# Kernel optimization log

Measured on AMD Instinct MI355X. Metric: run time of the kernel, lower is better.

The kernel has to match this reference:

```python
import jax, jax.numpy as jnp
import numpy as np

TOP_K = 2


def setup_inputs() -> dict:
    key = jax.random.key(0)
    ks = jax.random.split(key, 5)
    T, D, F, E = 2048, 2048, 7168, 8
    x = jax.random.normal(ks[0], (T, D), dtype=jnp.float32)
    gate_w = jax.random.normal(ks[1], (E, D), dtype=jnp.float32) * 0.02
    w1 = jax.random.normal(ks[2], (E, F, D), dtype=jnp.float32) * 0.02
    w3 = jax.random.normal(ks[3], (E, F, D), dtype=jnp.float32) * 0.02
    w2 = jax.random.normal(ks[4], (E, D, F), dtype=jnp.float32) * 0.02
    return {"x": x, "gate_w": gate_w, "w1": w1, "w3": w3, "w2": w2}


def reference(x, gate_w, w1, w3, w2):
    # x: (T, D); gate_w: (E, D); w1/w3: (E, F, D); w2: (E, D, F)
    T = x.shape[0]
    E = gate_w.shape[0]
    gate_logits = x @ gate_w.T                          # (T, E)
    all_probs = jax.nn.softmax(gate_logits.astype(jnp.float32), axis=-1)
    # keep only top-k probabilities (zero the rest), then renormalize
    top_vals, top_idx = jax.lax.top_k(all_probs, TOP_K)  # (T, k)
    rows = jnp.arange(T)[:, None]
    masked = jnp.zeros((T, E), dtype=jnp.float32).at[rows, top_idx].set(top_vals)
    weights = (masked / masked.sum(axis=1, keepdims=True)).astype(x.dtype)  # (T, E)
    # dense all-expert SwiGLU FFN, weighted accumulate
    g = jnp.einsum('td,efd->tef', x, w1)                # (T, E, F)
    u = jnp.einsum('td,efd->tef', x, w3)                # (T, E, F)
    h = jax.nn.silu(g) * u                              # (T, E, F)
    h = h * weights[:, :, None]
    out = jnp.einsum('tef,edf->td', h, w2)              # (T, D)
    return out
```

## Files before the change

kernel.cpp:

```cpp
#include <hip/hip_runtime.h>
#include <hip/hip_bf16.h>
#include <cstdint>
#include <cstddef>

#define TTOK 2048
#define DDIM 2048
#define FDIM 7168
#define NEXP 8
#define NMT (TTOK / 128)

typedef __attribute__((ext_vector_type(8))) short bf16x8;
typedef __attribute__((ext_vector_type(4))) float f32x4;

__device__ __forceinline__ unsigned short f2bf(float f) {
  __hip_bfloat16 h = __float2bfloat16(f);
  unsigned short s;
  __builtin_memcpy(&s, &h, 2);
  return s;
}

__device__ __forceinline__ ushort4 f2bf4(float4 v) {
  ushort4 o;
  o.x = f2bf(v.x); o.y = f2bf(v.y); o.z = f2bf(v.z); o.w = f2bf(v.w);
  return o;
}

__device__ __forceinline__ void gload_lds16(const void* g, void* l) {
  __builtin_amdgcn_global_load_lds((const __attribute__((address_space(1))) void*)g,
                                   (__attribute__((address_space(3))) void*)l,
                                   16, 0, 0);
}

__global__ void cvt_x_kernel(const float* __restrict__ x, unsigned short* __restrict__ xb, int n4) {
  int i = blockIdx.x * blockDim.x + threadIdx.x;
  if (i >= n4) return;
  ((ushort4*)xb)[i] = f2bf4(((const float4*)x)[i]);
}

__global__ void cvt_w_kernel(const float* __restrict__ src, unsigned short* __restrict__ dst, long n4) {
  const long stride = (long)gridDim.x * blockDim.x;
  long i = (long)blockIdx.x * blockDim.x + threadIdx.x;
  for (; i + 7 * stride < n4; i += 8 * stride) {
    float4 v[8];
    #pragma unroll
    for (int u = 0; u < 8; ++u) v[u] = ((const float4*)src)[i + u * stride];
    #pragma unroll
    for (int u = 0; u < 8; ++u) ((ushort4*)dst)[i + u * stride] = f2bf4(v[u]);
  }
  for (; i < n4; i += stride)
    ((ushort4*)dst)[i] = f2bf4(((const float4*)src)[i]);
}

__global__ void gate_kernel(const float* __restrict__ x, const float* __restrict__ gw,
                            int* __restrict__ counts, int* __restrict__ lists,
                            float* __restrict__ wrow) {
  const int wv = threadIdx.x >> 6, ln = threadIdx.x & 63;
  const int t = blockIdx.x * 4 + wv;
  float acc[8];
  #pragma unroll
  for (int e = 0; e < 8; ++e) acc[e] = 0.f;
  const float* xp = x + (size_t)t * DDIM;
  for (int d = ln; d < DDIM; d += 64) {
    float xv = xp[d];
    #pragma unroll
    for (int e = 0; e < 8; ++e) acc[e] += xv * gw[e * DDIM + d];
  }
  #pragma unroll
  for (int e = 0; e < 8; ++e) {
    float v = acc[e];
    #pragma unroll
    for (int off = 32; off > 0; off >>= 1) v += __shfl_down(v, off);
    acc[e] = v;
  }
  if (ln == 0) {
    int i0 = 0;
    #pragma unroll
    for (int e = 1; e < 8; ++e) if (acc[e] > acc[i0]) i0 = e;
    int i1 = (i0 == 0) ? 1 : 0;
    #pragma unroll
    for (int e = 0; e < 8; ++e) if (e != i0 && acc[e] > acc[i1]) i1 = e;
    float p1 = expf(acc[i1] - acc[i0]);
    float w0 = 1.f / (1.f + p1);
    float w1v = p1 / (1.f + p1);
    int pos0 = atomicAdd(&counts[i0], 1);
    lists[i0 * TTOK + pos0] = t; wrow[i0 * TTOK + pos0] = w0;
    int pos1 = atomicAdd(&counts[i1], 1);
    lists[i1 * TTOK + pos1] = t; wrow[i1 * TTOK + pos1] = w1v;
  }
}

__global__ void prefix_kernel(const int* __restrict__ counts, int* __restrict__ hoff) {
  if (threadIdx.x == 0) {
    int s = 0;
    for (int e = 0; e < NEXP; ++e) { hoff[e] = s; s += counts[e]; }
  }
}



__launch_bounds__(256, 2)
__global__ void gemm1b_kernel(const unsigned short* __restrict__ xb,
                              const unsigned short* __restrict__ w1b,
                              const unsigned short* __restrict__ w3b,
                              const int* __restrict__ counts,
                              const int* __restrict__ hoff,
                              const int* __restrict__ lists,
                              const float* __restrict__ wrow,
                              unsigned short* __restrict__ H) {
  const int ft = blockIdx.x, mt = blockIdx.y, e = blockIdx.z;
  const int cnt = counts[e];
  if (mt * 128 >= cnt) return;

  __shared__ __align__(16) unsigned short smA[128 * 64];
  __shared__ __align__(16) unsigned short smB1[128 * 64];
  __shared__ __align__(16) unsigned short smB3[128 * 64];
  __shared__ float smW[128];

  const int tid = threadIdx.x;
  const int wv = tid >> 6, ln = tid & 63;
  const int wr = wv >> 1, wc = wv & 1;

  if (tid < 128) {
    int pos = mt * 128 + tid;
    smW[tid] = (pos < cnt) ? wrow[e * TTOK + pos] : 0.f;
  }

  const int colSwz = (((ln & 7) ^ (ln >> 3)) * 8);
  const int rlocal = wv * 8 + (ln >> 3);

  const int* lst = lists + e * TTOK;
  const unsigned short* xap[4];
  #pragma unroll
  for (int q = 0; q < 4; ++q) {
    int pos = mt * 128 + q * 32 + rlocal;
    int tok = (pos < cnt) ? lst[pos] : 0;
    xap[q] = xb + (size_t)tok * DDIM + colSwz;
  }
  const size_t eoff = (size_t)e * FDIM * DDIM;
  const unsigned short* b1p[4];
  const unsigned short* b3p[4];
  #pragma unroll
  for (int q = 0; q < 4; ++q) {
    size_t row = (size_t)(ft * 128 + q * 32 + rlocal);
    b1p[q] = w1b + eoff + row * DDIM + colSwz;
    b3p[q] = w3b + eoff + row * DDIM + colSwz;
  }

  f32x4 accG[4][4], accU[4][4];
  #pragma unroll
  for (int i = 0; i < 4; ++i)
    #pragma unroll
    for (int j = 0; j < 4; ++j) {
      accG[i][j] = (f32x4){0.f, 0.f, 0.f, 0.f};
      accU[i][j] = (f32x4){0.f, 0.f, 0.f, 0.f};
    }

  const int NKT = DDIM / 64;
  for (int kt = 0; kt < NKT; ++kt) {
    #pragma unroll
    for (int q = 0; q < 4; ++q) {
      gload_lds16(xap[q] + kt * 64, (char*)smA  + q * 4096 + wv * 1024);
      gload_lds16(b1p[q] + kt * 64, (char*)smB1 + q * 4096 + wv * 1024);
      gload_lds16(b3p[q] + kt * 64, (char*)smB3 + q * 4096 + wv * 1024);
    }
    __syncthreads();

    #pragma unroll
    for (int kk = 0; kk < 2; ++kk) {
      const int phys = ((kk * 4 + (ln >> 4)) ^ (ln & 7)) * 8;
      bf16x8 af[4], b1f[4], b3f[4];
      #pragma unroll
      for (int mi = 0; mi < 4; ++mi)
        af[mi] = *(const bf16x8*)(smA + (wr * 64 + mi * 16 + (ln & 15)) * 64 + phys);
      #pragma unroll
      for (int ni = 0; ni < 4; ++ni) {
        b1f[ni] = *(const bf16x8*)(smB1 + (wc * 64 + ni * 16 + (ln & 15)) * 64 + phys);
        b3f[ni] = *(const bf16x8*)(smB3 + (wc * 64 + ni * 16 + (ln & 15)) * 64 + phys);
      }
      #pragma unroll
      for (int mi = 0; mi < 4; ++mi)
        #pragma unroll
        for (int ni = 0; ni < 4; ++ni) {
          accG[mi][ni] = __builtin_amdgcn_mfma_f32_16x16x32_bf16(af[mi], b1f[ni], accG[mi][ni], 0, 0, 0);
          accU[mi][ni] = __builtin_amdgcn_mfma_f32_16x16x32_bf16(af[mi], b3f[ni], accU[mi][ni], 0, 0, 0);
        }
    }
    __syncthreads();
  }

  const int hbase = hoff[e];
  #pragma unroll
  for (int mi = 0; mi < 4; ++mi) {
    #pragma unroll
    for (int ni = 0; ni < 4; ++ni) {
      int col = ft * 128 + wc * 64 + ni * 16 + (ln & 15);
      #pragma unroll
      for (int r = 0; r < 4; ++r) {
        int rl = wr * 64 + mi * 16 + (ln >> 4) * 4 + r;
        int pos = mt * 128 + rl;
        if (pos < cnt) {
          float g = accG[mi][ni][r], u = accU[mi][ni][r];
          float s = g / (1.f + expf(-g));
          H[(size_t)(hbase + pos) * FDIM + col] = f2bf(s * u * smW[rl]);
        }
      }
    }
  }
}

__launch_bounds__(256, 2)
__global__ void gemm2b_kernel(const unsigned short* __restrict__ H,
                              const unsigned short* __restrict__ w2b,
                              const int* __restrict__ counts,
                              const int* __restrict__ hoff,
                              const int* __restrict__ lists,
                              float* __restrict__ out) {
  const int nt = blockIdx.x, e = blockIdx.z;
  const int mt = blockIdx.y >> 1, khalf = blockIdx.y & 1;
  const int cnt = counts[e];
  if (mt * 128 >= cnt) return;

  __shared__ __align__(16) unsigned short smA[128 * 64];
  __shared__ __align__(16) unsigned short smB[128 * 64];
  __shared__ int smTok[128];

  const int tid = threadIdx.x;
  const int wv = tid >> 6, ln = tid & 63;
  const int wr = wv >> 1, wc = wv & 1;

  if (tid < 128) {
    int pos = mt * 128 + tid;
    smTok[tid] = (pos < cnt) ? lists[e * TTOK + pos] : -1;
  }

  const int colSwz = (((ln & 7) ^ (ln >> 3)) * 8);
  const int rlocal = wv * 8 + (ln >> 3);
  const int hbase = hoff[e];
  const int kofs = khalf * (FDIM / 2);

  const unsigned short* hap[4];
  const unsigned short* b2p[4];
  #pragma unroll
  for (int q = 0; q < 4; ++q) {
    hap[q] = H + (size_t)(hbase + mt * 128 + q * 32 + rlocal) * FDIM + kofs + colSwz;
    b2p[q] = w2b + (size_t)e * DDIM * FDIM + (size_t)(nt * 128 + q * 32 + rlocal) * FDIM + kofs + colSwz;
  }

  f32x4 acc[4][4];
  #pragma unroll
  for (int i = 0; i < 4; ++i)
    #pragma unroll
    for (int j = 0; j < 4; ++j) acc[i][j] = (f32x4){0.f, 0.f, 0.f, 0.f};

  const int NKT = FDIM / 2 / 64;
  for (int kt = 0; kt < NKT; ++kt) {
    #pragma unroll
    for (int q = 0; q < 4; ++q) {
      gload_lds16(hap[q] + kt * 64, (char*)smA + q * 4096 + wv * 1024);
      gload_lds16(b2p[q] + kt * 64, (char*)smB + q * 4096 + wv * 1024);
    }
    __syncthreads();

    #pragma unroll
    for (int kk = 0; kk < 2; ++kk) {
      const int phys = ((kk * 4 + (ln >> 4)) ^ (ln & 7)) * 8;
      bf16x8 af[4], bf[4];
      #pragma unroll
      for (int mi = 0; mi < 4; ++mi)
        af[mi] = *(const bf16x8*)(smA + (wr * 64 + mi * 16 + (ln & 15)) * 64 + phys);
      #pragma unroll
      for (int ni = 0; ni < 4; ++ni)
        bf[ni] = *(const bf16x8*)(smB + (wc * 64 + ni * 16 + (ln & 15)) * 64 + phys);
      #pragma unroll
      for (int mi = 0; mi < 4; ++mi)
        #pragma unroll
        for (int ni = 0; ni < 4; ++ni)
          acc[mi][ni] = __builtin_amdgcn_mfma_f32_16x16x32_bf16(af[mi], bf[ni], acc[mi][ni], 0, 0, 0);
    }
    __syncthreads();
  }

  #pragma unroll
  for (int mi = 0; mi < 4; ++mi) {
    #pragma unroll
    for (int ni = 0; ni < 4; ++ni) {
      int col = nt * 128 + wc * 64 + ni * 16 + (ln & 15);
      #pragma unroll
      for (int r = 0; r < 4; ++r) {
        int rl = wr * 64 + mi * 16 + (ln >> 4) * 4 + r;
        int tok = smTok[rl];
        if (tok >= 0) atomicAdd(out + (size_t)tok * DDIM + col, acc[mi][ni][r]);
      }
    }
  }
}


__launch_bounds__(256, 2)
__global__ void gemm1_kernel(const unsigned short* __restrict__ xb,
                             const float* __restrict__ w1,
                             const float* __restrict__ w3,
                             const int* __restrict__ counts,
                             const int* __restrict__ hoff,
                             const int* __restrict__ lists,
                             const float* __restrict__ wrow,
                             unsigned short* __restrict__ H) {
  const int ft = blockIdx.x, mt = blockIdx.y, e = blockIdx.z;
  const int cnt = counts[e];
  if (mt * 128 >= cnt) return;

  __shared__ __align__(16) unsigned short smA[128 * 64];
  __shared__ __align__(16) unsigned short smB1[128 * 64];
  __shared__ __align__(16) unsigned short smB3[128 * 64];
  __shared__ float smW[128];

  const int tid = threadIdx.x;
  const int wv = tid >> 6, ln = tid & 63;
  const int wr = wv >> 1, wc = wv & 1;

  if (tid < 128) {
    int pos = mt * 128 + tid;
    smW[tid] = (pos < cnt) ? wrow[e * TTOK + pos] : 0.f;
  }

  const int* lst = lists + e * TTOK;
  const int colA = (((ln & 7) ^ (ln >> 3)) * 8);
  const unsigned short* xap[4];
  #pragma unroll
  for (int q = 0; q < 4; ++q) {
    int pos = mt * 128 + q * 32 + wv * 8 + (ln >> 3);
    int tok = (pos < cnt) ? lst[pos] : 0;
    xap[q] = xb + (size_t)tok * DDIM + colA;
  }

  const int rowB = tid >> 1;
  const int halfB = tid & 1;
  const size_t eoff = (size_t)e * FDIM * DDIM;
  const float* w1p = w1 + eoff + (size_t)(ft * 128 + rowB) * DDIM + halfB * 32;
  const float* w3p = w3 + eoff + (size_t)(ft * 128 + rowB) * DDIM + halfB * 32;
  int physB[4];
  #pragma unroll
  for (int q = 0; q < 4; ++q) physB[q] = ((halfB * 4 + q) ^ (rowB & 7)) * 8;

  float4 bv1[8], bv3[8];
  f32x4 accG[4][4], accU[4][4];
  #pragma unroll
  for (int i = 0; i < 4; ++i)
    #pragma unroll
    for (int j = 0; j < 4; ++j) {
      accG[i][j] = (f32x4){0.f, 0.f, 0.f, 0.f};
      accU[i][j] = (f32x4){0.f, 0.f, 0.f, 0.f};
    }

  #define STAGE_A(KT) do { \
    _Pragma("unroll") \
    for (int q = 0; q < 4; ++q) \
      gload_lds16(xap[q] + (KT) * 64, (char*)smA + q * 4096 + wv * 1024); \
  } while (0)
  #define LOAD_B(KT) do { \
    _Pragma("unroll") \
    for (int q = 0; q < 8; ++q) bv1[q] = *(const float4*)(w1p + (KT) * 64 + q * 4); \
    _Pragma("unroll") \
    for (int q = 0; q < 8; ++q) bv3[q] = *(const float4*)(w3p + (KT) * 64 + q * 4); \
  } while (0)
  #define STORE_B() do { \
    _Pragma("unroll") \
    for (int q = 0; q < 4; ++q) { \
      bf16x8 t1, t3; \
      float4 a0 = bv1[2 * q], a1 = bv1[2 * q + 1]; \
      t1[0] = (short)f2bf(a0.x); t1[1] = (short)f2bf(a0.y); t1[2] = (short)f2bf(a0.z); t1[3] = (short)f2bf(a0.w); \
      t1[4] = (short)f2bf(a1.x); t1[5] = (short)f2bf(a1.y); t1[6] = (short)f2bf(a1.z); t1[7] = (short)f2bf(a1.w); \
      float4 c0 = bv3[2 * q], c1 = bv3[2 * q + 1]; \
      t3[0] = (short)f2bf(c0.x); t3[1] = (short)f2bf(c0.y); t3[2] = (short)f2bf(c0.z); t3[3] = (short)f2bf(c0.w); \
      t3[4] = (short)f2bf(c1.x); t3[5] = (short)f2bf(c1.y); t3[6] = (short)f2bf(c1.z); t3[7] = (short)f2bf(c1.w); \
      *(bf16x8*)(smB1 + rowB * 64 + physB[q]) = t1; \
      *(bf16x8*)(smB3 + rowB * 64 + physB[q]) = t3; \
    } \
  } while (0)

  STAGE_A(0);
  LOAD_B(0);
  STORE_B();
  __syncthreads();

  const int NKT = DDIM / 64;
  for (int kt = 0; kt < NKT; ++kt) {
    if (kt < NKT - 1) {
      LOAD_B(kt + 1);
      __builtin_amdgcn_sched_barrier(0);
    }
    #pragma unroll
    for (int kk = 0; kk < 2; ++kk) {
      const int phys = ((kk * 4 + (ln >> 4)) ^ (ln & 7)) * 8;
      bf16x8 af[4], b1f[4], b3f[4];
      #pragma unroll
      for (int mi = 0; mi < 4; ++mi)
        af[mi] = *(const bf16x8*)(smA + (wr * 64 + mi * 16 + (ln & 15)) * 64 + phys);
      #pragma unroll
      for (int ni = 0; ni < 4; ++ni) {
        b1f[ni] = *(const bf16x8*)(smB1 + (wc * 64 + ni * 16 + (ln & 15)) * 64 + phys);
        b3f[ni] = *(const bf16x8*)(smB3 + (wc * 64 + ni * 16 + (ln & 15)) * 64 + phys);
      }
      #pragma unroll
      for (int mi = 0; mi < 4; ++mi)
        #pragma unroll
        for (int ni = 0; ni < 4; ++ni) {
          accG[mi][ni] = __builtin_amdgcn_mfma_f32_16x16x32_bf16(af[mi], b1f[ni], accG[mi][ni], 0, 0, 0);
          accU[mi][ni] = __builtin_amdgcn_mfma_f32_16x16x32_bf16(af[mi], b3f[ni], accU[mi][ni], 0, 0, 0);
        }
    }
    if (kt == NKT - 1) break;
    __syncthreads();
    STORE_B();
    STAGE_A(kt + 1);
    __syncthreads();
  }

  const int hbase = hoff[e];
  #pragma unroll
  for (int mi = 0; mi < 4; ++mi) {
    #pragma unroll
    for (int ni = 0; ni < 4; ++ni) {
      int col = ft * 128 + wc * 64 + ni * 16 + (ln & 15);
      #pragma unroll
      for (int r = 0; r < 4; ++r) {
        int rl = wr * 64 + mi * 16 + (ln >> 4) * 4 + r;
        int pos = mt * 128 + rl;
        if (pos < cnt) {
          float g = accG[mi][ni][r], u = accU[mi][ni][r];
          float s = g / (1.f + expf(-g));
          H[(size_t)(hbase + pos) * FDIM + col] = f2bf(s * u * smW[rl]);
        }
      }
    }
  }
  #undef STAGE_A
  #undef LOAD_B
  #undef STORE_B
}

__launch_bounds__(256, 2)
__global__ void gemm2_kernel(const unsigned short* __restrict__ H,
                             const float* __restrict__ w2,
                             const int* __restrict__ counts,
                             const int* __restrict__ hoff,
                             const int* __restrict__ lists,
                             float* __restrict__ out) {
  const int nt = blockIdx.x, mt = blockIdx.y, e = blockIdx.z;
  const int cnt = counts[e];
  if (mt * 128 >= cnt) return;

  __shared__ __align__(16) unsigned short smA[128 * 64];
  __shared__ __align__(16) unsigned short smB[128 * 64];
  __shared__ int smTok[128];

  const int tid = threadIdx.x;
  const int wv = tid >> 6, ln = tid & 63;
  const int wr = wv >> 1, wc = wv & 1;

  if (tid < 128) {
    int pos = mt * 128 + tid;
    smTok[tid] = (pos < cnt) ? lists[e * TTOK + pos] : -1;
  }

  const int hbase = hoff[e];
  const int colA = (((ln & 7) ^ (ln >> 3)) * 8);
  const unsigned short* hap[4];
  #pragma unroll
  for (int q = 0; q < 4; ++q)
    hap[q] = H + (size_t)(hbase + mt * 128 + q * 32 + wv * 8 + (ln >> 3)) * FDIM + colA;

  const int rowB = tid >> 1;
  const int halfB = tid & 1;
  const float* w2p = w2 + (size_t)e * DDIM * FDIM + (size_t)(nt * 128 + rowB) * FDIM + halfB * 32;
  int physB[4];
  #pragma unroll
  for (int q = 0; q < 4; ++q) physB[q] = ((halfB * 4 + q) ^ (rowB & 7)) * 8;

  float4 bv[8];
  f32x4 acc[4][4];
  #pragma unroll
  for (int i = 0; i < 4; ++i)
    #pragma unroll
    for (int j = 0; j < 4; ++j) acc[i][j] = (f32x4){0.f, 0.f, 0.f, 0.f};

  #define STAGE_A2(KT) do { \
    _Pragma("unroll") \
    for (int q = 0; q < 4; ++q) \
      gload_lds16(hap[q] + (KT) * 64, (char*)smA + q * 4096 + wv * 1024); \
  } while (0)
  #define LOAD_B2(KT) do { \
    _Pragma("unroll") \
    for (int q = 0; q < 8; ++q) bv[q] = *(const float4*)(w2p + (KT) * 64 + q * 4); \
  } while (0)
  #define STORE_B2() do { \
    _Pragma("unroll") \
    for (int q = 0; q < 4; ++q) { \
      bf16x8 t; \
      float4 a0 = bv[2 * q], a1 = bv[2 * q + 1]; \
      t[0] = (short)f2bf(a0.x); t[1] = (short)f2bf(a0.y); t[2] = (short)f2bf(a0.z); t[3] = (short)f2bf(a0.w); \
      t[4] = (short)f2bf(a1.x); t[5] = (short)f2bf(a1.y); t[6] = (short)f2bf(a1.z); t[7] = (short)f2bf(a1.w); \
      *(bf16x8*)(smB + rowB * 64 + physB[q]) = t; \
    } \
  } while (0)

  STAGE_A2(0);
  LOAD_B2(0);
  STORE_B2();
  __syncthreads();

  const int NKT = FDIM / 64;
  for (int kt = 0; kt < NKT; ++kt) {
    if (kt < NKT - 1) {
      LOAD_B2(kt + 1);
      __builtin_amdgcn_sched_barrier(0);
    }
    #pragma unroll
    for (int kk = 0; kk < 2; ++kk) {
      const int phys = ((kk * 4 + (ln >> 4)) ^ (ln & 7)) * 8;
      bf16x8 af[4], bf[4];
      #pragma unroll
      for (int mi = 0; mi < 4; ++mi)
        af[mi] = *(const bf16x8*)(smA + (wr * 64 + mi * 16 + (ln & 15)) * 64 + phys);
      #pragma unroll
      for (int ni = 0; ni < 4; ++ni)
        bf[ni] = *(const bf16x8*)(smB + (wc * 64 + ni * 16 + (ln & 15)) * 64 + phys);
      #pragma unroll
      for (int mi = 0; mi < 4; ++mi)
        #pragma unroll
        for (int ni = 0; ni < 4; ++ni)
          acc[mi][ni] = __builtin_amdgcn_mfma_f32_16x16x32_bf16(af[mi], bf[ni], acc[mi][ni], 0, 0, 0);
    }
    if (kt == NKT - 1) break;
    __syncthreads();
    STORE_B2();
    STAGE_A2(kt + 1);
    __syncthreads();
  }

  #pragma unroll
  for (int mi = 0; mi < 4; ++mi) {
    #pragma unroll
    for (int ni = 0; ni < 4; ++ni) {
      int col = nt * 128 + wc * 64 + ni * 16 + (ln & 15);
      #pragma unroll
      for (int r = 0; r < 4; ++r) {
        int rl = wr * 64 + mi * 16 + (ln >> 4) * 4 + r;
        int tok = smTok[rl];
        if (tok >= 0) atomicAdd(out + (size_t)tok * DDIM + col, acc[mi][ni][r]);
      }
    }
  }
  #undef STAGE_A2
  #undef LOAD_B2
  #undef STORE_B2
}

extern "C" void kernel_launch(void* const* d_in, const int* in_sizes, int n_in,
                              void* d_out, int out_size, void* d_ws, size_t ws_size,
                              hipStream_t stream) {
  const float* x  = (const float*)d_in[0];
  const float* gw = (const float*)d_in[1];
  const float* w1 = (const float*)d_in[2];
  const float* w3 = (const float*)d_in[3];
  const float* w2 = (const float*)d_in[4];
  float* out = (float*)d_out;
  char* ws = (char*)d_ws;

  const size_t XB_BYTES = (size_t)TTOK * DDIM * 2;
  const size_t H_BYTES  = (size_t)(2 * TTOK + 128) * FDIM * 2;
  const size_t W_ELEMS  = (size_t)NEXP * FDIM * DDIM;
  const size_t WB_BYTES = W_ELEMS * 2;
  const size_t META_BYTES = (size_t)NEXP * TTOK * 4 * 2 + 128;

  unsigned short* xb = (unsigned short*)ws;
  unsigned short* H  = (unsigned short*)(ws + XB_BYTES);

  const size_t need_bf16 = XB_BYTES + H_BYTES + 3 * WB_BYTES + META_BYTES;
  const bool use_bf16w = (ws_size >= need_bf16);

  char* p;
  unsigned short *w1b = nullptr, *w3b = nullptr, *w2b = nullptr;
  if (use_bf16w) {
    w1b = (unsigned short*)(ws + XB_BYTES + H_BYTES);
    w3b = (unsigned short*)((char*)w1b + WB_BYTES);
    w2b = (unsigned short*)((char*)w3b + WB_BYTES);
    p = (char*)w2b + WB_BYTES;
  } else {
    p = ws + XB_BYTES + H_BYTES;
  }
  int*   lists  = (int*)p;          p += NEXP * TTOK * 4;
  float* wrow   = (float*)p;        p += NEXP * TTOK * 4;
  int*   counts = (int*)p;          p += 64;
  int*   hoff   = (int*)p;

  hipMemsetAsync(d_out, 0, (size_t)TTOK * DDIM * 4, stream);
  hipMemsetAsync(counts, 0, NEXP * 4, stream);

  cvt_x_kernel<<<(TTOK * DDIM / 4 + 255) / 256, 256, 0, stream>>>(x, xb, TTOK * DDIM / 4);
  gate_kernel<<<TTOK / 4, 256, 0, stream>>>(x, gw, counts, lists, wrow);
  prefix_kernel<<<1, 64, 0, stream>>>(counts, hoff);

  if (use_bf16w) {
    const long n4 = (long)(W_ELEMS / 4);
    cvt_w_kernel<<<4096, 256, 0, stream>>>(w1, w1b, n4);
    cvt_w_kernel<<<4096, 256, 0, stream>>>(w3, w3b, n4);
    cvt_w_kernel<<<4096, 256, 0, stream>>>(w2, w2b, n4);
    gemm1b_kernel<<<dim3(FDIM / 128, NMT, NEXP), 256, 0, stream>>>(
        xb, w1b, w3b, counts, hoff, lists, wrow, H);
    gemm2b_kernel<<<dim3(DDIM / 128, 2 * NMT, NEXP), 256, 0, stream>>>(
        H, w2b, counts, hoff, lists, out);
  } else {
    gemm1_kernel<<<dim3(FDIM / 128, NMT, NEXP), 256, 0, stream>>>(
        xb, w1, w3, counts, hoff, lists, wrow, H);
    gemm2_kernel<<<dim3(DDIM / 128, NMT, NEXP), 256, 0, stream>>>(
        H, w2, counts, hoff, lists, out);
  }
}
```

Before: 1.118 ms.

## Double-buffer weight tiles in both expert GEMMs to overlap loads with MFMA

```diff
diff --git a/kernel.cpp b/kernel.cpp
--- a/kernel.cpp
+++ b/kernel.cpp
@@ -29,6 +29,13 @@
   __builtin_amdgcn_global_load_lds((const __attribute__((address_space(1))) void*)g,
                                    (__attribute__((address_space(3))) void*)l,
                                    16, 0, 0);
+}
+
+__device__ __forceinline__ void lds_barrier() {
+  asm volatile("s_waitcnt lgkmcnt(0)" ::: "memory");
+  __builtin_amdgcn_sched_barrier(0);
+  __builtin_amdgcn_s_barrier();
+  __builtin_amdgcn_sched_barrier(0);
 }
 
 __global__ void cvt_x_kernel(const float* __restrict__ x, unsigned short* __restrict__ xb, int n4) {
@@ -112,18 +119,12 @@
   if (mt * 128 >= cnt) return;
 
   __shared__ __align__(16) unsigned short smA[128 * 64];
-  __shared__ __align__(16) unsigned short smB1[128 * 64];
-  __shared__ __align__(16) unsigned short smB3[128 * 64];
-  __shared__ float smW[128];
+  __shared__ __align__(16) unsigned short smB1[2][128 * 64];
+  __shared__ __align__(16) unsigned short smB3[2][128 * 64];
 
   const int tid = threadIdx.x;
   const int wv = tid >> 6, ln = tid & 63;
   const int wr = wv >> 1, wc = wv & 1;
-
-  if (tid < 128) {
-    int pos = mt * 128 + tid;
-    smW[tid] = (pos < cnt) ? wrow[e * TTOK + pos] : 0.f;
-  }
 
   const int colSwz = (((ln & 7) ^ (ln >> 3)) * 8);
   const int rlocal = wv * 8 + (ln >> 3);
@@ -155,15 +156,25 @@
       accU[i][j] = (f32x4){0.f, 0.f, 0.f, 0.f};
     }
 
+  #pragma unroll
+  for (int q = 0; q < 4; ++q) {
+    gload_lds16(xap[q], (char*)smA + q * 4096 + wv * 1024);
+    gload_lds16(b1p[q], (char*)smB1[0] + q * 4096 + wv * 1024);
+    gload_lds16(b3p[q], (char*)smB3[0] + q * 4096 + wv * 1024);
+  }
+  __syncthreads();
+
   const int NKT = DDIM / 64;
   for (int kt = 0; kt < NKT; ++kt) {
-    #pragma unroll
-    for (int q = 0; q < 4; ++q) {
-      gload_lds16(xap[q] + kt * 64, (char*)smA  + q * 4096 + wv * 1024);
-      gload_lds16(b1p[q] + kt * 64, (char*)smB1 + q * 4096 + wv * 1024);
-      gload_lds16(b3p[q] + kt * 64, (char*)smB3 + q * 4096 + wv * 1024);
-    }
-    __syncthreads();
+    const int cur = kt & 1;
+    if (kt < NKT - 1) {
+      #pragma unroll
+      for (int q = 0; q < 4; ++q) {
+        gload_lds16(b1p[q] + (kt + 1) * 64, (char*)smB1[cur ^ 1] + q * 4096 + wv * 1024);
+        gload_lds16(b3p[q] + (kt + 1) * 64, (char*)smB3[cur ^ 1] + q * 4096 + wv * 1024);
+      }
+      __builtin_amdgcn_sched_barrier(0);
+    }
 
     #pragma unroll
     for (int kk = 0; kk < 2; ++kk) {
@@ -174,8 +185,8 @@
         af[mi] = *(const bf16x8*)(smA + (wr * 64 + mi * 16 + (ln & 15)) * 64 + phys);
       #pragma unroll
       for (int ni = 0; ni < 4; ++ni) {
-        b1f[ni] = *(const bf16x8*)(smB1 + (wc * 64 + ni * 16 + (ln & 15)) * 64 + phys);
-        b3f[ni] = *(const bf16x8*)(smB3 + (wc * 64 + ni * 16 + (ln & 15)) * 64 + phys);
+        b1f[ni] = *(const bf16x8*)(smB1[cur] + (wc * 64 + ni * 16 + (ln & 15)) * 64 + phys);
+        b3f[ni] = *(const bf16x8*)(smB3[cur] + (wc * 64 + ni * 16 + (ln & 15)) * 64 + phys);
       }
       #pragma unroll
       for (int mi = 0; mi < 4; ++mi)
@@ -185,6 +196,12 @@
           accU[mi][ni] = __builtin_amdgcn_mfma_f32_16x16x32_bf16(af[mi], b3f[ni], accU[mi][ni], 0, 0, 0);
         }
     }
+    if (kt == NKT - 1) break;
+
+    lds_barrier();
+    #pragma unroll
+    for (int q = 0; q < 4; ++q)
+      gload_lds16(xap[q] + (kt + 1) * 64, (char*)smA + q * 4096 + wv * 1024);
     __syncthreads();
   }
 
@@ -201,7 +218,8 @@
         if (pos < cnt) {
           float g = accG[mi][ni][r], u = accU[mi][ni][r];
           float s = g / (1.f + expf(-g));
-          H[(size_t)(hbase + pos) * FDIM + col] = f2bf(s * u * smW[rl]);
+          float wt = wrow[e * TTOK + pos];
+          H[(size_t)(hbase + pos) * FDIM + col] = f2bf(s * u * wt);
         }
       }
     }
@@ -221,7 +239,7 @@
   if (mt * 128 >= cnt) return;
 
   __shared__ __align__(16) unsigned short smA[128 * 64];
-  __shared__ __align__(16) unsigned short smB[128 * 64];
+  __shared__ __align__(16) unsigned short smB[2][128 * 64];
   __shared__ int smTok[128];
 
   const int tid = threadIdx.x;
@@ -252,14 +270,22 @@
     #pragma unroll
     for (int j = 0; j < 4; ++j) acc[i][j] = (f32x4){0.f, 0.f, 0.f, 0.f};
 
+  #pragma unroll
+  for (int q = 0; q < 4; ++q) {
+    gload_lds16(hap[q], (char*)smA + q * 4096 + wv * 1024);
+    gload_lds16(b2p[q], (char*)smB[0] + q * 4096 + wv * 1024);
+  }
+  __syncthreads();
+
   const int NKT = FDIM / 2 / 64;
   for (int kt = 0; kt < NKT; ++kt) {
-    #pragma unroll
-    for (int q = 0; q < 4; ++q) {
-      gload_lds16(hap[q] + kt * 64, (char*)smA + q * 4096 + wv * 1024);
-      gload_lds16(b2p[q] + kt * 64, (char*)smB + q * 4096 + wv * 1024);
-    }
-    __syncthreads();
+    const int cur = kt & 1;
+    if (kt < NKT - 1) {
+      #pragma unroll
+      for (int q = 0; q < 4; ++q)
+        gload_lds16(b2p[q] + (kt + 1) * 64, (char*)smB[cur ^ 1] + q * 4096 + wv * 1024);
+      __builtin_amdgcn_sched_barrier(0);
+    }
 
     #pragma unroll
     for (int kk = 0; kk < 2; ++kk) {
@@ -270,13 +296,19 @@
         af[mi] = *(const bf16x8*)(smA + (wr * 64 + mi * 16 + (ln & 15)) * 64 + phys);
       #pragma unroll
       for (int ni = 0; ni < 4; ++ni)
-        bf[ni] = *(const bf16x8*)(smB + (wc * 64 + ni * 16 + (ln & 15)) * 64 + phys);
+        bf[ni] = *(const bf16x8*)(smB[cur] + (wc * 64 + ni * 16 + (ln & 15)) * 64 + phys);
       #pragma unroll
       for (int mi = 0; mi < 4; ++mi)
         #pragma unroll
         for (int ni = 0; ni < 4; ++ni)
           acc[mi][ni] = __builtin_amdgcn_mfma_f32_16x16x32_bf16(af[mi], bf[ni], acc[mi][ni], 0, 0, 0);
     }
+    if (kt == NKT - 1) break;
+
+    lds_barrier();
+    #pragma unroll
+    for (int q = 0; q < 4; ++q)
+      gload_lds16(hap[q] + (kt + 1) * 64, (char*)smA + q * 4096 + wv * 1024);
     __syncthreads();
   }
 
```

New measurement: 1.166 ms. +4.3%, slower.
